# Optimization experiments

Hardware: AMD Instinct MI355X
Metric: run time of the kernel (lower is better)

The kernel has to match this reference:

```python
import jax, jax.numpy as jnp
import numpy as np

B, T, E, H = 2, 2048, 1024, 16
D = E // H  # head_dim = 64


def setup_inputs() -> dict:
    key = jax.random.key(0)
    kx, kq, kk, kv, ko = jax.random.split(key, 5)
    x = jax.random.normal(kx, (B, T, E), dtype=jnp.float32)
    # nn.Parameter(torch.randn(...)) -> standard normal params
    Wq = jax.random.normal(kq, (H, E, D), dtype=jnp.float32)
    Wk = jax.random.normal(kk, (H, E, D), dtype=jnp.float32)
    Wv = jax.random.normal(kv, (H, E, D), dtype=jnp.float32)
    # nn.Linear(E, E, bias=False): weight [out, in], y = a @ Wo.T
    Wo = jax.random.normal(ko, (E, E), dtype=jnp.float32) * (1.0 / np.sqrt(E))
    # boolean mask: True positions are filled with -inf (causal: strict upper tri)
    mask = jnp.triu(jnp.ones((T, T), dtype=bool), k=1)
    return {"x": x, "mask": mask, "Wq": Wq, "Wk": Wk, "Wv": Wv, "Wo": Wo}


def reference(x, mask, Wq, Wk, Wv, Wo):
    # x: [b, t, e]; Wq/Wk/Wv: [h, e, i]
    q = jnp.einsum('hei,bte->hbti', Wq, x)
    k = jnp.einsum('hei,bte->hbti', Wk, x)
    v = jnp.einsum('hei,bte->hbti', Wv, x)
    # NOTE: original scales by sqrt(seq_len) (x.shape[1]), not sqrt(head_dim)
    scale = x.shape[1] ** 0.5
    fit = jnp.einsum('hbti,hbTi->hbtT', q, k) / scale  # [h, b, t, T]
    fit = jnp.where(mask, -jnp.inf, fit)
    p = jax.nn.softmax(fit, axis=-1)
    att = jnp.einsum('hbtT,hbTi->hbti', p, v)          # [h, b, t, i]
    # rearrange 'h b t i -> b t (h i)'
    b, t = att.shape[1], att.shape[2]
    att = jnp.transpose(att, (1, 2, 0, 3)).reshape(b, t, -1)
    return att @ Wo.T
```

## Files before the change

### kernel.cpp

```cpp
#include <hip/hip_runtime.h>
#include <hip/hip_fp8.h>
#include <stdint.h>

constexpr float INV_SCALE = 0.022097086912079608f;
constexpr float LOG2E = 1.4426950408889634f;
constexpr float QSC = INV_SCALE * LOG2E;

typedef __attribute__((ext_vector_type(8))) short bfrag;
typedef __attribute__((ext_vector_type(4))) float facc;
typedef __attribute__((ext_vector_type(4))) unsigned short us4;

#define MFMA(a, b, c) __builtin_amdgcn_mfma_f32_16x16x32_bf16((a), (b), (c), 0, 0, 0)
#define EXP2(x) __builtin_amdgcn_exp2f(x)

__device__ __forceinline__ unsigned short f2bh(float f) {
    union { float f; unsigned int u; } cv; cv.f = f;
    unsigned int u = cv.u;
    u += 0x7FFFu + ((u >> 16) & 1u);
    return (unsigned short)(u >> 16);
}
__device__ __forceinline__ float bh2f(unsigned short h) {
    union { unsigned int u; float f; } cv; cv.u = ((unsigned int)h) << 16;
    return cv.f;
}
__device__ __forceinline__ void gl_lds16(const unsigned short* g, unsigned short* lds) {
    __builtin_amdgcn_global_load_lds(
        (const __attribute__((address_space(1))) unsigned int*)g,
        (__attribute__((address_space(3))) unsigned int*)lds, 16, 0, 0);
}
__device__ __forceinline__ bfrag f8frag(uint2 raw) {
    union { uint2 u; unsigned char b[8]; } cv; cv.u = raw;
    bfrag r;
    #pragma unroll
    for (int j = 0; j < 8; ++j) {
        const __hip_fp8_e4m3* t = reinterpret_cast<const __hip_fp8_e4m3*>(&cv.b[j]);
        r[j] = (short)f2bh((float)(*t) * 0.00390625f);
    }
    return r;
}

__global__ __launch_bounds__(256) void x_split(const float* __restrict__ x,
                                               unsigned short* __restrict__ xh,
                                               unsigned short* __restrict__ xl) {
    int idx = blockIdx.x * 256 + threadIdx.x;
    facc v = *(const facc*)&x[(size_t)idx * 4];
    us4 hv, lv;
    #pragma unroll
    for (int j = 0; j < 4; ++j) {
        unsigned short hb = f2bh(v[j]);
        hv[j] = hb;
        lv[j] = f2bh(v[j] - bh2f(hb));
    }
    *(us4*)&xh[(size_t)idx * 4] = hv;
    *(us4*)&xl[(size_t)idx * 4] = lv;
}

__global__ __launch_bounds__(256) void prep_w(
    const float* __restrict__ Wq, const float* __restrict__ Wk, const float* __restrict__ Wv,
    unsigned short* __restrict__ WqTh, unsigned short* __restrict__ WqTl,
    unsigned short* __restrict__ WkTh, unsigned short* __restrict__ WkTl,
    unsigned short* __restrict__ WvT)
{
    __shared__ float tile[64][65];
    const int tid = threadIdx.x;
    const int et = blockIdx.x, h = blockIdx.y, m = blockIdx.z;
    const float* W = (m == 0) ? Wq : (m == 1) ? Wk : Wv;
    #pragma unroll
    for (int rep = 0; rep < 4; ++rep) {
        int idx = rep * 256 + tid;
        int e = idx >> 4, i4 = (idx & 15) * 4;
        facc v = *(const facc*)&W[(size_t)h * 65536 + (size_t)(et * 64 + e) * 64 + i4];
        tile[e][i4] = v.x; tile[e][i4 + 1] = v.y; tile[e][i4 + 2] = v.z; tile[e][i4 + 3] = v.w;
    }
    __syncthreads();
    unsigned short* Oh = (m == 0) ? WqTh : (m == 1) ? WkTh : WvT;
    unsigned short* Ol = (m == 0) ? WqTl : WkTl;
    #pragma unroll
    for (int rep = 0; rep < 4; ++rep) {
        int idx = rep * 256 + tid;
        int i = idx >> 4, e4 = (idx & 15) * 4;
        us4 hv, lv;
        #pragma unroll
        for (int j = 0; j < 4; ++j) {
            float f = tile[e4 + j][i];
            unsigned short hb = f2bh(f);
            hv[j] = hb;
            lv[j] = f2bh(f - bh2f(hb));
        }
        size_t o = (size_t)(h * 64 + i) * 1024 + et * 64 + e4;
        *(us4*)&Oh[o] = hv;
        if (m < 2) *(us4*)&Ol[o] = lv;
    }
}

__global__ __launch_bounds__(256) void wo_conv(const float* __restrict__ Wo,
                                               unsigned short* __restrict__ WoB) {
    int idx = blockIdx.x * 256 + threadIdx.x;
    facc v = *(const facc*)&Wo[(size_t)idx * 4];
    us4 o;
    #pragma unroll
    for (int j = 0; j < 4; ++j) o[j] = f2bh(v[j]);
    *(us4*)&WoB[(size_t)idx * 4] = o;
}

__global__ __launch_bounds__(512, 2) void qkv_fused(
    const unsigned short* __restrict__ xh, const unsigned short* __restrict__ xl,
    const unsigned short* __restrict__ WqTh, const unsigned short* __restrict__ WqTl,
    const unsigned short* __restrict__ WkTh, const unsigned short* __restrict__ WkTl,
    const unsigned short* __restrict__ WvT,
    unsigned short* __restrict__ qh, unsigned char* __restrict__ ql8,
    unsigned short* __restrict__ kh, unsigned short* __restrict__ kl,
    unsigned short* __restrict__ vT)
{
    extern __shared__ unsigned short sm[];
    unsigned short* Ab = sm;
    unsigned short* Qb = sm + 16384;
    unsigned short* Kb = sm + 32768;
    unsigned short* Vb = sm + 49152;
    const int tid = threadIdx.x;
    const int w = tid >> 6, l = tid & 63;
    const int wm = w >> 2, wn = w & 3;
    const int ct = blockIdx.x, rt = blockIdx.y;

    const int lc = (l & 7) ^ (l >> 3);
    const int krel = (lc & 3) * 8;
    const unsigned short* Axp = (lc < 4) ? xh : xl;
    const unsigned short* Qp  = (lc < 4) ? WqTh : WqTl;
    const unsigned short* Kp  = (lc < 4) ? WkTh : WkTl;

    facc accq[4][2], acck[4][2], accv[4][2];
    #pragma unroll
    for (int m = 0; m < 4; ++m)
        #pragma unroll
        for (int n = 0; n < 2; ++n) {
            accq[m][n] = (facc)(0.0f); acck[m][n] = (facc)(0.0f); accv[m][n] = (facc)(0.0f);
        }

    auto stageAB = [&](int buf, int e0) {
        #pragma unroll
        for (int i = 0; i < 2; ++i) {
            int slice = w * 2 + i;
            int row = slice * 8 + (l >> 3);
            size_t sa = (size_t)(rt * 128 + row) * 1024 + e0 + krel;
            size_t sb = (size_t)(ct * 128 + row) * 1024 + e0 + krel;
            gl_lds16(&Axp[sa], &Ab[buf * 8192 + slice * 512]);
            gl_lds16(&Qp[sb],  &Qb[buf * 8192 + slice * 512]);
            gl_lds16(&Kp[sb],  &Kb[buf * 8192 + slice * 512]);
        }
    };

    stageAB(0, 0);
    #pragma unroll
    for (int i = 0; i < 2; ++i) {
        int slice = w * 2 + i;
        int row = slice * 8 + (l >> 3);
        gl_lds16(&WvT[(size_t)(ct * 128 + row) * 1024 + lc * 8], &Vb[slice * 512]);
    }
    asm volatile("s_waitcnt vmcnt(0)" ::: "memory");
    __builtin_amdgcn_s_barrier();

    for (int t = 0; t < 32; ++t) {
        __builtin_amdgcn_s_barrier();
        __builtin_amdgcn_sched_barrier(0);
        if (t < 31) stageAB((t + 1) & 1, (t + 1) * 32);
        {
            int wv = (t >> 1) + 1;
            if (wv < 16) {
                int slice = w + (t & 1) * 8;
                int row = slice * 8 + (l >> 3);
                gl_lds16(&WvT[(size_t)(ct * 128 + row) * 1024 + wv * 64 + lc * 8],
                         &Vb[(wv & 1) * 8192 + slice * 512]);
            }
        }
        __builtin_amdgcn_sched_barrier(0);
        if (t < 30)       asm volatile("s_waitcnt vmcnt(7)" ::: "memory");
        else if (t == 30) asm volatile("s_waitcnt vmcnt(6)" ::: "memory");
        else              asm volatile("s_waitcnt vmcnt(0)" ::: "memory");
        __builtin_amdgcn_sched_barrier(0);
        __builtin_amdgcn_s_barrier();
        __builtin_amdgcn_sched_barrier(0);

        const unsigned short* Ac = &Ab[(t & 1) * 8192];
        const unsigned short* Qc = &Qb[(t & 1) * 8192];
        const unsigned short* Kc = &Kb[(t & 1) * 8192];
        const unsigned short* Vc = &Vb[((t >> 1) & 1) * 8192];
        const int ca = (l >> 4) ^ (l & 7);
        const int cb = ca ^ 4;
        const int cv = ca ^ ((t & 1) << 2);

        bfrag afh[4], afl[4];
        #pragma unroll
        for (int m = 0; m < 4; ++m) {
            int row = wm * 64 + m * 16 + (l & 15);
            afh[m] = *(const bfrag*)&Ac[row * 64 + ca * 8];
            afl[m] = *(const bfrag*)&Ac[row * 64 + cb * 8];
        }
        #pragma unroll
        for (int n = 0; n < 2; ++n) {
            int nr = wn * 32 + n * 16 + (l & 15);
            bfrag bv = *(const bfrag*)&Vc[nr * 64 + cv * 8];
            #pragma unroll
            for (int m = 0; m < 4; ++m) accv[m][n] = MFMA(afh[m], bv, accv[m][n]);
        }
        #pragma unroll
        for (int n = 0; n < 2; ++n) {
            int nr = wn * 32 + n * 16 + (l & 15);
            bfrag bh = *(const bfrag*)&Qc[nr * 64 + ca * 8];
            bfrag bl = *(const bfrag*)&Qc[nr * 64 + cb * 8];
            #pragma unroll
            for (int m = 0; m < 4; ++m) {
                accq[m][n] = MFMA(afh[m], bh, accq[m][n]);
                accq[m][n] = MFMA(afh[m], bl, accq[m][n]);
                accq[m][n] = MFMA(afl[m], bh, accq[m][n]);
            }
        }
        #pragma unroll
        for (int n = 0; n < 2; ++n) {
            int nr = wn * 32 + n * 16 + (l & 15);
            bfrag bh = *(const bfrag*)&Kc[nr * 64 + ca * 8];
            bfrag bl = *(const bfrag*)&Kc[nr * 64 + cb * 8];
            #pragma unroll
            for (int m = 0; m < 4; ++m) {
                acck[m][n] = MFMA(afh[m], bh, acck[m][n]);
                acck[m][n] = MFMA(afh[m], bl, acck[m][n]);
                acck[m][n] = MFMA(afl[m], bh, acck[m][n]);
            }
        }
    }

    #pragma unroll
    for (int m = 0; m < 4; ++m)
        #pragma unroll
        for (int r = 0; r < 4; ++r) {
            int row = rt * 128 + wm * 64 + m * 16 + (l >> 4) * 4 + r;
            #pragma unroll
            for (int n = 0; n < 2; ++n) {
                int col = ct * 128 + wn * 32 + n * 16 + (l & 15);
                float fq = accq[m][n][r] * QSC;
                unsigned short hb = f2bh(fq);
                qh[(size_t)row * 1024 + col] = hb;
                __hip_fp8_e4m3 e((fq - bh2f(hb)) * 256.0f);
                ql8[(size_t)row * 1024 + col] = *reinterpret_cast<unsigned char*>(&e);
                float fk = acck[m][n][r];
                unsigned short kb = f2bh(fk);
                kh[(size_t)row * 1024 + col] = kb;
                kl[(size_t)row * 1024 + col] = f2bh(fk - bh2f(kb));
            }
        }
    #pragma unroll
    for (int m = 0; m < 4; ++m) {
        int t0g = rt * 128 + wm * 64 + m * 16 + (l >> 4) * 4;
        int b_ = t0g >> 11, t0 = t0g & 2047;
        #pragma unroll
        for (int n = 0; n < 2; ++n) {
            int col = ct * 128 + wn * 32 + n * 16 + (l & 15);
            int h_ = col >> 6, d = col & 63;
            us4 pk;
            #pragma unroll
            for (int r = 0; r < 4; ++r) pk[r] = f2bh(accv[m][n][r]);
            *(us4*)&vT[((size_t)((h_ * 2 + b_) * 64 + d)) * 2048 + t0] = pk;
        }
    }
}

__device__ __forceinline__ void stage_kv(
    const unsigned short* __restrict__ kh, const unsigned short* __restrict__ kl,
    const unsigned short* __restrict__ vT,
    unsigned short* Khb, unsigned short* Klb, unsigned short* Vtb,
    int w, int l, int b, int h, int kt)
{
    #pragma unroll
    for (int i = 0; i < 2; ++i) {
        int pbase = (w * 2 + i) * 1024;
        int p = pbase + l * 16;
        int row = p >> 7, slot = (p >> 4) & 7;
        int chunk = slot ^ (row & 7);
        size_t srcK = (size_t)(b * 2048 + kt * 64 + row) * 1024 + h * 64 + chunk * 8;
        size_t srcV = ((size_t)(h * 2 + b) * 64 + row) * 2048 + (size_t)kt * 64 + chunk * 8;
        gl_lds16(&kh[srcK], &Khb[pbase >> 1]);
        gl_lds16(&kl[srcK], &Klb[pbase >> 1]);
        gl_lds16(&vT[srcV], &Vtb[pbase >> 1]);
    }
}

__device__ __forceinline__ void attn_step(
    const unsigned short* Khb, const unsigned short* Klb, const unsigned short* Vtb,
    unsigned short* Pl, const bfrag* qfh, const bfrag* qfl,
    facc* O, float* mrow, float* lrow, int w, int l, bool diag)
{
    facc S[4];
    #pragma unroll
    for (int f = 0; f < 4; ++f) S[f] = (facc)(0.0f);
    #pragma unroll
    for (int s = 0; s < 2; ++s) {
        #pragma unroll
        for (int f = 0; f < 4; ++f) {
            int key = f * 16 + (l & 15);
            int ch = (s * 4 + (l >> 4)) ^ (key & 7);
            bfrag kbh = *(const bfrag*)&Khb[key * 64 + ch * 8];
            bfrag kbl = *(const bfrag*)&Klb[key * 64 + ch * 8];
            S[f] = MFMA(qfh[s], kbh, S[f]);
            S[f] = MFMA(qfh[s], kbl, S[f]);
            S[f] = MFMA(qfl[s], kbh, S[f]);
        }
    }
    if (diag) {
        #pragma unroll
        for (int f = 0; f < 4; ++f) {
            int keyl = f * 16 + (l & 15);
            #pragma unroll
            for (int r = 0; r < 4; ++r) {
                int qls = w * 16 + (l >> 4) * 4 + r;
                if (keyl > qls) S[f][r] = -1e30f;
            }
        }
    }
    #pragma unroll
    for (int r = 0; r < 4; ++r) {
        float mx = fmaxf(fmaxf(S[0][r], S[1][r]), fmaxf(S[2][r], S[3][r]));
        mx = fmaxf(mx, __shfl_xor(mx, 1));
        mx = fmaxf(mx, __shfl_xor(mx, 2));
        mx = fmaxf(mx, __shfl_xor(mx, 4));
        mx = fmaxf(mx, __shfl_xor(mx, 8));
        float mn = fmaxf(mrow[r], mx);
        float fac = EXP2(mrow[r] - mn);
        mrow[r] = mn;
        float rs = 0.0f;
        #pragma unroll
        for (int f = 0; f < 4; ++f) { S[f][r] = EXP2(S[f][r] - mn); rs += S[f][r]; }
        rs += __shfl_xor(rs, 1); rs += __shfl_xor(rs, 2);
        rs += __shfl_xor(rs, 4); rs += __shfl_xor(rs, 8);
        lrow[r] = lrow[r] * fac + rs;
        O[0][r] *= fac; O[1][r] *= fac; O[2][r] *= fac; O[3][r] *= fac;
    }
    #pragma unroll
    for (int f = 0; f < 4; ++f) {
        int key = f * 16 + (l & 15);
        #pragma unroll
        for (int r = 0; r < 4; ++r) {
            int qr = w * 16 + (l >> 4) * 4 + r;
            Pl[qr * 64 + (((key >> 3) ^ (qr & 7)) * 8) + (key & 7)] = f2bh(S[f][r]);
        }
    }
    #pragma unroll
    for (int s = 0; s < 2; ++s) {
        int qa = w * 16 + (l & 15);
        int cha = (s * 4 + (l >> 4)) ^ (qa & 7);
        bfrag pa = *(const bfrag*)&Pl[qa * 64 + cha * 8];
        #pragma unroll
        for (int f = 0; f < 4; ++f) {
            int d = f * 16 + (l & 15);
            int chv = (s * 4 + (l >> 4)) ^ (d & 7);
            bfrag vb = *(const bfrag*)&Vtb[d * 64 + chv * 8];
            O[f] = MFMA(pa, vb, O[f]);
        }
    }
}

__global__ __launch_bounds__(256, 2) void attn_mfma(
    const unsigned short* __restrict__ qh, const unsigned char* __restrict__ ql8,
    const unsigned short* __restrict__ kh, const unsigned short* __restrict__ kl,
    const unsigned short* __restrict__ vT, unsigned short* __restrict__ att)
{
    __shared__ unsigned short Kh[2][64 * 64], Kl[2][64 * 64], Vt[2][64 * 64], Pl[64 * 64];
    const int tid = threadIdx.x, w = tid >> 6, l = tid & 63;
    const int dd = blockIdx.y * 16 + blockIdx.x;
    const int xcd = dd & 7, sl = dd >> 3;
    const int hb = xcd * 4 + (sl >> 4);
    const int bx = sl & 15;
    const int qtA = 31 - bx, qtB = bx;
    const int h = hb >> 1, b = hb & 1;

    bfrag qfhA[2], qflA[2], qfhB[2], qflB[2];
    {
        const int qrowA = qtA * 64 + w * 16 + (l & 15);
        const size_t qoffA = (size_t)(b * 2048 + qrowA) * 1024 + h * 64 + (l >> 4) * 8;
        qfhA[0] = *(const bfrag*)&qh[qoffA];
        qfhA[1] = *(const bfrag*)&qh[qoffA + 32];
        qflA[0] = f8frag(*(const uint2*)&ql8[qoffA]);
        qflA[1] = f8frag(*(const uint2*)&ql8[qoffA + 32]);
        const int qrowB = qtB * 64 + w * 16 + (l & 15);
        const size_t qoffB = (size_t)(b * 2048 + qrowB) * 1024 + h * 64 + (l >> 4) * 8;
        qfhB[0] = *(const bfrag*)&qh[qoffB];
        qfhB[1] = *(const bfrag*)&qh[qoffB + 32];
        qflB[0] = f8frag(*(const uint2*)&ql8[qoffB]);
        qflB[1] = f8frag(*(const uint2*)&ql8[qoffB + 32]);
    }

    facc OA[4], OB[4];
    float mA[4], lA[4], mB[4], lB[4];
    #pragma unroll
    for (int f = 0; f < 4; ++f) { OA[f] = (facc)(0.0f); OB[f] = (facc)(0.0f); }
    #pragma unroll
    for (int r = 0; r < 4; ++r) { mA[r] = -1e30f; lA[r] = 0.0f; mB[r] = -1e30f; lB[r] = 0.0f; }

    stage_kv(kh, kl, vT, Kh[0], Kl[0], Vt[0], w, l, b, h, 0);
    int cur = 0;
    for (int kt = 0; kt <= qtA; ++kt) {
        __syncthreads();
        if (kt < qtA)
            stage_kv(kh, kl, vT, Kh[cur ^ 1], Kl[cur ^ 1], Vt[cur ^ 1], w, l, b, h, kt + 1);
        __builtin_amdgcn_sched_barrier(0);
        __builtin_amdgcn_s_barrier();
        __builtin_amdgcn_sched_barrier(0);
        attn_step(Kh[cur], Kl[cur], Vt[cur], Pl, qfhA, qflA, OA, mA, lA, w, l, kt == qtA);
        if (kt <= qtB)
            attn_step(Kh[cur], Kl[cur], Vt[cur], Pl, qfhB, qflB, OB, mB, lB, w, l, kt == qtB);
        cur ^= 1;
    }

    #pragma unroll
    for (int f = 0; f < 4; ++f) {
        int d = h * 64 + f * 16 + (l & 15);
        #pragma unroll
        for (int r = 0; r < 4; ++r) {
            int tA = qtA * 64 + w * 16 + (l >> 4) * 4 + r;
            att[(size_t)(b * 2048 + tA) * 1024 + d] = f2bh(OA[f][r] / lA[r]);
            int tB = qtB * 64 + w * 16 + (l >> 4) * 4 + r;
            att[(size_t)(b * 2048 + tB) * 1024 + d] = f2bh(OB[f][r] / lB[r]);
        }
    }
}

__global__ __launch_bounds__(256, 2) void outproj(
    const unsigned short* __restrict__ att, const unsigned short* __restrict__ WoB,
    float* __restrict__ out)
{
    __shared__ unsigned short Ab[2][128 * 64], Bb[2][128 * 64];
    const int tid = threadIdx.x, w = tid >> 6, l = tid & 63;
    const int wm = w >> 1, wn = w & 1;
    const int rt = blockIdx.x, ct = blockIdx.y;

    const int lc = (l & 7) ^ (l >> 3);
    facc acc[4][4];
    #pragma unroll
    for (int i = 0; i < 4; ++i)
        #pragma unroll
        for (int j = 0; j < 4; ++j) acc[i][j] = (facc)(0.0f);

    auto stage = [&](int buf, int e0) {
        #pragma unroll
        for (int i = 0; i < 4; ++i) {
            int slice = w * 4 + i;
            int row = slice * 8 + (l >> 3);
            gl_lds16(&att[(size_t)(rt * 128 + row) * 1024 + e0 + lc * 8], &Ab[buf][slice * 512]);
            gl_lds16(&WoB[(size_t)(ct * 128 + row) * 1024 + e0 + lc * 8], &Bb[buf][slice * 512]);
        }
    };

    stage(0, 0);
    int cur = 0;
    for (int t = 0; t < 16; ++t) {
        __syncthreads();
        if (t < 15) stage(cur ^ 1, (t + 1) * 64);
        __builtin_amdgcn_sched_barrier(0);
        __builtin_amdgcn_s_barrier();
        __builtin_amdgcn_sched_barrier(0);
        #pragma unroll
        for (int s = 0; s < 2; ++s) {
            const int slot = (s * 4 + (l >> 4)) ^ (l & 7);
            bfrag af[4], bf_[4];
            #pragma unroll
            for (int m = 0; m < 4; ++m)
                af[m] = *(const bfrag*)&Ab[cur][(wm * 64 + m * 16 + (l & 15)) * 64 + slot * 8];
            #pragma unroll
            for (int n = 0; n < 4; ++n)
                bf_[n] = *(const bfrag*)&Bb[cur][(wn * 64 + n * 16 + (l & 15)) * 64 + slot * 8];
            #pragma unroll
            for (int m = 0; m < 4; ++m)
                #pragma unroll
                for (int n = 0; n < 4; ++n)
                    acc[m][n] = MFMA(af[m], bf_[n], acc[m][n]);
        }
        cur ^= 1;
    }
    #pragma unroll
    for (int m = 0; m < 4; ++m)
        #pragma unroll
        for (int r = 0; r < 4; ++r) {
            int row = rt * 128 + wm * 64 + m * 16 + (l >> 4) * 4 + r;
            #pragma unroll
            for (int n = 0; n < 4; ++n) {
                int col = ct * 128 + wn * 64 + n * 16 + (l & 15);
                out[(size_t)row * 1024 + col] = acc[m][n][r];
            }
        }
}

extern "C" void kernel_launch(void* const* d_in, const int* in_sizes, int n_in,
                              void* d_out, int out_size, void* d_ws, size_t ws_size,
                              hipStream_t stream) {
    const float* x  = (const float*)d_in[0];
    const float* Wq = (const float*)d_in[2];
    const float* Wk = (const float*)d_in[3];
    const float* Wv = (const float*)d_in[4];
    const float* Wo = (const float*)d_in[5];

    uint8_t* wsb = (uint8_t*)d_ws;
    const size_t MB = 1024 * 1024;
    unsigned short* WqTh = (unsigned short*)(wsb + 0 * MB);
    unsigned short* WqTl = (unsigned short*)(wsb + 2 * MB);
    unsigned short* WkTh = (unsigned short*)(wsb + 4 * MB);
    unsigned short* WkTl = (unsigned short*)(wsb + 6 * MB);
    unsigned short* WvT  = (unsigned short*)(wsb + 8 * MB);
    unsigned short* qh   = (unsigned short*)(wsb + 10 * MB);
    unsigned char*  ql8  = (unsigned char*)(wsb + 18 * MB);
    unsigned short* kh   = (unsigned short*)(wsb + 22 * MB);
    unsigned short* kl   = (unsigned short*)(wsb + 30 * MB);
    unsigned short* vT   = (unsigned short*)(wsb + 38 * MB);
    unsigned short* att  = (unsigned short*)(wsb + 46 * MB);
    unsigned short* xh   = (unsigned short*)(wsb + 46 * MB);
    unsigned short* WoB  = (unsigned short*)(wsb + 54 * MB);
    unsigned short* xl   = (unsigned short*)(wsb + 56 * MB);

    hipFuncSetAttribute((const void*)qkv_fused,
                        hipFuncAttributeMaxDynamicSharedMemorySize, 131072);

    x_split<<<dim3(4096), 256, 0, stream>>>(x, xh, xl);
    prep_w<<<dim3(16, 16, 3), 256, 0, stream>>>(Wq, Wk, Wv, WqTh, WqTl, WkTh, WkTl, WvT);
    wo_conv<<<dim3(1024), 256, 0, stream>>>(Wo, WoB);
    qkv_fused<<<dim3(8, 32), 512, 131072, stream>>>(xh, xl, WqTh, WqTl, WkTh, WkTl, WvT,
                                                    qh, ql8, kh, kl, vT);
    attn_mfma<<<dim3(16, 32), 256, 0, stream>>>(qh, ql8, kh, kl, vT, att);
    outproj<<<dim3(32, 8), 256, 0, stream>>>(att, WoB, (float*)d_out);
}
```

Before: 172.9 us.

## Lazy softmax rescale, MFMA row sums, setprio, and merge Wo/x prep kernels

The attention step now skips the running-max rescale of the output accumulators unless some row's max grew by more than a threshold (checked wave-wide). It also computes the softmax denominator with an extra MFMA against a ones vector instead of shuffle reductions. MFMA sections are wrapped in s_setprio to favour matrix issue. The x split and Wo bf16 conversion kernels are merged into one launch to save a launch. The changes trade a little extra MFMA work and a possible divergence check for fewer exp/shuffle/VALU operations; the lazy rescale relies on bounded exponent growth for accuracy.

Measured after the change: 167.9 us. 1.03x faster.

```diff
diff --git a/kernel.cpp b/kernel.cpp
--- a/kernel.cpp
+++ b/kernel.cpp
@@ -39,20 +39,31 @@
     return r;
 }
 
-__global__ __launch_bounds__(256) void x_split(const float* __restrict__ x,
+__global__ __launch_bounds__(256) void prep_xw(const float* __restrict__ x,
+                                               const float* __restrict__ Wo,
                                                unsigned short* __restrict__ xh,
-                                               unsigned short* __restrict__ xl) {
-    int idx = blockIdx.x * 256 + threadIdx.x;
-    facc v = *(const facc*)&x[(size_t)idx * 4];
-    us4 hv, lv;
-    #pragma unroll
-    for (int j = 0; j < 4; ++j) {
-        unsigned short hb = f2bh(v[j]);
-        hv[j] = hb;
-        lv[j] = f2bh(v[j] - bh2f(hb));
-    }
-    *(us4*)&xh[(size_t)idx * 4] = hv;
-    *(us4*)&xl[(size_t)idx * 4] = lv;
+                                               unsigned short* __restrict__ xl,
+                                               unsigned short* __restrict__ WoB) {
+    if (blockIdx.x < 1024) {
+        int idx = blockIdx.x * 256 + threadIdx.x;
+        facc v = *(const facc*)&Wo[(size_t)idx * 4];
+        us4 o;
+        #pragma unroll
+        for (int j = 0; j < 4; ++j) o[j] = f2bh(v[j]);
+        *(us4*)&WoB[(size_t)idx * 4] = o;
+    } else {
+        int idx = (blockIdx.x - 1024) * 256 + threadIdx.x;
+        facc v = *(const facc*)&x[(size_t)idx * 4];
+        us4 hv, lv;
+        #pragma unroll
+        for (int j = 0; j < 4; ++j) {
+            unsigned short hb = f2bh(v[j]);
+            hv[j] = hb;
+            lv[j] = f2bh(v[j] - bh2f(hb));
+        }
+        *(us4*)&xh[(size_t)idx * 4] = hv;
+        *(us4*)&xl[(size_t)idx * 4] = lv;
+    }
 }
 
 __global__ __launch_bounds__(256) void prep_w(
@@ -91,16 +102,6 @@
         *(us4*)&Oh[o] = hv;
         if (m < 2) *(us4*)&Ol[o] = lv;
     }
-}
-
-__global__ __launch_bounds__(256) void wo_conv(const float* __restrict__ Wo,
-                                               unsigned short* __restrict__ WoB) {
-    int idx = blockIdx.x * 256 + threadIdx.x;
-    facc v = *(const facc*)&Wo[(size_t)idx * 4];
-    us4 o;
-    #pragma unroll
-    for (int j = 0; j < 4; ++j) o[j] = f2bh(v[j]);
-    *(us4*)&WoB[(size_t)idx * 4] = o;
 }
 
 __global__ __launch_bounds__(512, 2) void qkv_fused(
@@ -286,11 +287,12 @@
 __device__ __forceinline__ void attn_step(
     const unsigned short* Khb, const unsigned short* Klb, const unsigned short* Vtb,
     unsigned short* Pl, const bfrag* qfh, const bfrag* qfl,
-    facc* O, float* mrow, float* lrow, int w, int l, bool diag)
+    facc* O, facc& Osum, float* mrow, bfrag ones, int w, int l, bool diag)
 {
     facc S[4];
     #pragma unroll
     for (int f = 0; f < 4; ++f) S[f] = (facc)(0.0f);
+    __builtin_amdgcn_s_setprio(1);
     #pragma unroll
     for (int s = 0; s < 2; ++s) {
         #pragma unroll
@@ -304,6 +306,7 @@
             S[f] = MFMA(qfl[s], kbh, S[f]);
         }
     }
+    __builtin_amdgcn_s_setprio(0);
     if (diag) {
         #pragma unroll
         for (int f = 0; f < 4; ++f) {
@@ -315,24 +318,32 @@
             }
         }
     }
+    float mx[4];
+    float dmax = -3.0e38f;
     #pragma unroll
     for (int r = 0; r < 4; ++r) {
-        float mx = fmaxf(fmaxf(S[0][r], S[1][r]), fmaxf(S[2][r], S[3][r]));
-        mx = fmaxf(mx, __shfl_xor(mx, 1));
-        mx = fmaxf(mx, __shfl_xor(mx, 2));
-        mx = fmaxf(mx, __shfl_xor(mx, 4));
-        mx = fmaxf(mx, __shfl_xor(mx, 8));
-        float mn = fmaxf(mrow[r], mx);
-        float fac = EXP2(mrow[r] - mn);
-        mrow[r] = mn;
-        float rs = 0.0f;
-        #pragma unroll
-        for (int f = 0; f < 4; ++f) { S[f][r] = EXP2(S[f][r] - mn); rs += S[f][r]; }
-        rs += __shfl_xor(rs, 1); rs += __shfl_xor(rs, 2);
-        rs += __shfl_xor(rs, 4); rs += __shfl_xor(rs, 8);
-        lrow[r] = lrow[r] * fac + rs;
-        O[0][r] *= fac; O[1][r] *= fac; O[2][r] *= fac; O[3][r] *= fac;
-    }
+        float m0 = fmaxf(fmaxf(S[0][r], S[1][r]), fmaxf(S[2][r], S[3][r]));
+        m0 = fmaxf(m0, __shfl_xor(m0, 1));
+        m0 = fmaxf(m0, __shfl_xor(m0, 2));
+        m0 = fmaxf(m0, __shfl_xor(m0, 4));
+        m0 = fmaxf(m0, __shfl_xor(m0, 8));
+        mx[r] = m0;
+        dmax = fmaxf(dmax, m0 - mrow[r]);
+    }
+    if (!__all(dmax <= 8.0f)) {
+        #pragma unroll
+        for (int r = 0; r < 4; ++r) {
+            float mn = fmaxf(mrow[r], mx[r]);
+            float fac = EXP2(mrow[r] - mn);
+            mrow[r] = mn;
+            O[0][r] *= fac; O[1][r] *= fac; O[2][r] *= fac; O[3][r] *= fac;
+            Osum[r] *= fac;
+        }
+    }
+    #pragma unroll
+    for (int r = 0; r < 4; ++r)
+        #pragma unroll
+        for (int f = 0; f < 4; ++f) S[f][r] = EXP2(S[f][r] - mrow[r]);
     #pragma unroll
     for (int f = 0; f < 4; ++f) {
         int key = f * 16 + (l & 15);
@@ -342,11 +353,13 @@
             Pl[qr * 64 + (((key >> 3) ^ (qr & 7)) * 8) + (key & 7)] = f2bh(S[f][r]);
         }
     }
+    __builtin_amdgcn_s_setprio(1);
     #pragma unroll
     for (int s = 0; s < 2; ++s) {
         int qa = w * 16 + (l & 15);
         int cha = (s * 4 + (l >> 4)) ^ (qa & 7);
         bfrag pa = *(const bfrag*)&Pl[qa * 64 + cha * 8];
+        Osum = MFMA(pa, ones, Osum);
         #pragma unroll
         for (int f = 0; f < 4; ++f) {
             int d = f * 16 + (l & 15);
@@ -355,6 +368,7 @@
             O[f] = MFMA(pa, vb, O[f]);
         }
     }
+    __builtin_amdgcn_s_setprio(0);
 }
 
 __global__ __launch_bounds__(256, 2) void attn_mfma(
@@ -362,7 +376,7 @@
     const unsigned short* __restrict__ kh, const unsigned short* __restrict__ kl,
     const unsigned short* __restrict__ vT, unsigned short* __restrict__ att)
 {
-    __shared__ unsigned short Kh[2][64 * 64], Kl[2][64 * 64], Vt[2][64 * 64], Pl[64 * 64];
+    __shared__ unsigned short Kh[2][4096], Kl[2][4096], Vt[2][4096], Pl[4096];
     const int tid = threadIdx.x, w = tid >> 6, l = tid & 63;
     const int dd = blockIdx.y * 16 + blockIdx.x;
     const int xcd = dd & 7, sl = dd >> 3;
@@ -370,6 +384,10 @@
     const int bx = sl & 15;
     const int qtA = 31 - bx, qtB = bx;
     const int h = hb >> 1, b = hb & 1;
+
+    bfrag ones;
+    #pragma unroll
+    for (int j = 0; j < 8; ++j) ones[j] = (short)0x3F80;
 
     bfrag qfhA[2], qflA[2], qfhB[2], qflB[2];
     {
@@ -387,26 +405,28 @@
         qflB[1] = f8frag(*(const uint2*)&ql8[qoffB + 32]);
     }
 
-    facc OA[4], OB[4];
-    float mA[4], lA[4], mB[4], lB[4];
+    facc OA[4], OB[4], OsA, OsB;
+    float mA[4], mB[4];
     #pragma unroll
     for (int f = 0; f < 4; ++f) { OA[f] = (facc)(0.0f); OB[f] = (facc)(0.0f); }
-    #pragma unroll
-    for (int r = 0; r < 4; ++r) { mA[r] = -1e30f; lA[r] = 0.0f; mB[r] = -1e30f; lB[r] = 0.0f; }
+    OsA = (facc)(0.0f); OsB = (facc)(0.0f);
+    #pragma unroll
+    for (int r = 0; r < 4; ++r) { mA[r] = -1e30f; mB[r] = -1e30f; }
 
     stage_kv(kh, kl, vT, Kh[0], Kl[0], Vt[0], w, l, b, h, 0);
-    int cur = 0;
     for (int kt = 0; kt <= qtA; ++kt) {
+        const int cur = kt & 1;
         __syncthreads();
         if (kt < qtA)
             stage_kv(kh, kl, vT, Kh[cur ^ 1], Kl[cur ^ 1], Vt[cur ^ 1], w, l, b, h, kt + 1);
         __builtin_amdgcn_sched_barrier(0);
         __builtin_amdgcn_s_barrier();
         __builtin_amdgcn_sched_barrier(0);
-        attn_step(Kh[cur], Kl[cur], Vt[cur], Pl, qfhA, qflA, OA, mA, lA, w, l, kt == qtA);
+        attn_step(Kh[cur], Kl[cur], Vt[cur], Pl, qfhA, qflA, OA, OsA, mA, ones,
+                  w, l, kt == qtA);
         if (kt <= qtB)
-            attn_step(Kh[cur], Kl[cur], Vt[cur], Pl, qfhB, qflB, OB, mB, lB, w, l, kt == qtB);
-        cur ^= 1;
+            attn_step(Kh[cur], Kl[cur], Vt[cur], Pl, qfhB, qflB, OB, OsB, mB, ones,
+                      w, l, kt == qtB);
     }
 
     #pragma unroll
@@ -415,9 +435,9 @@
         #pragma unroll
         for (int r = 0; r < 4; ++r) {
             int tA = qtA * 64 + w * 16 + (l >> 4) * 4 + r;
-            att[(size_t)(b * 2048 + tA) * 1024 + d] = f2bh(OA[f][r] / lA[r]);
+            att[(size_t)(b * 2048 + tA) * 1024 + d] = f2bh(OA[f][r] / OsA[r]);
             int tB = qtB * 64 + w * 16 + (l >> 4) * 4 + r;
-            att[(size_t)(b * 2048 + tB) * 1024 + d] = f2bh(OB[f][r] / lB[r]);
+            att[(size_t)(b * 2048 + tB) * 1024 + d] = f2bh(OB[f][r] / OsB[r]);
         }
     }
 }
@@ -516,9 +536,8 @@
     hipFuncSetAttribute((const void*)qkv_fused,
                         hipFuncAttributeMaxDynamicSharedMemorySize, 131072);
 
-    x_split<<<dim3(4096), 256, 0, stream>>>(x, xh, xl);
+    prep_xw<<<dim3(5120), 256, 0, stream>>>(x, Wo, xh, xl, WoB);
     prep_w<<<dim3(16, 16, 3), 256, 0, stream>>>(Wq, Wk, Wv, WqTh, WqTl, WkTh, WkTl, WvT);
-    wo_conv<<<dim3(1024), 256, 0, stream>>>(Wo, WoB);
     qkv_fused<<<dim3(8, 32), 512, 131072, stream>>>(xh, xl, WqTh, WqTl, WkTh, WkTl, WvT,
                                                     qh, ql8, kh, kl, vT);
     attn_mfma<<<dim3(16, 32), 256, 0, stream>>>(qh, ql8, kh, kl, vT, att);
```
